# Kernel tuning notes

Measured on AMD Instinct MI355X. Metric: run time of the kernel, lower is better.

## Reference

```python
import jax, jax.numpy as jnp
import numpy as np

N_NODES = 100000
N_EDGES = 1600000
N_GRAPHS = 1024
HID = 128
NODE_DIM = 7
EDGE_DIM = 3
LAYERS = 4
LN_EPS = 1e-5


def setup_inputs() -> dict:
    key = jax.random.key(0)
    ks = jax.random.split(key, 24)
    s = lambda i, shape, scale=0.05: (jax.random.normal(ks[i], shape, dtype=jnp.float32) * scale)
    x = jax.random.normal(ks[0], (N_NODES, NODE_DIM), dtype=jnp.float32)
    edge_index = jax.random.randint(ks[1], (2, N_EDGES), 0, N_NODES, dtype=jnp.int32)
    edge_attr = jax.random.normal(ks[2], (N_EDGES, EDGE_DIM), dtype=jnp.float32)
    batch = jnp.sort(jax.random.randint(ks[3], (N_NODES,), 0, N_GRAPHS, dtype=jnp.int32))
    return {
        'x': x, 'edge_index': edge_index, 'edge_attr': edge_attr, 'batch': batch,
        'inW': s(4, (NODE_DIM, HID)), 'inb': s(5, (HID,)),
        'edgeW': s(6, (LAYERS, EDGE_DIM, HID)), 'edgeb': s(7, (LAYERS, HID)),
        'w1': s(8, (LAYERS, HID, HID)), 'b1': s(9, (LAYERS, HID)),
        'w2': s(10, (LAYERS, HID, HID)), 'b2': s(11, (LAYERS, HID)),
        'gamma': jnp.ones((LAYERS, HID), dtype=jnp.float32),
        'beta': jnp.zeros((LAYERS, HID), dtype=jnp.float32),
        'fcW1': s(12, (HID, HID)), 'fcb1': s(13, (HID,)),
        'fcW2': s(14, (HID, HID // 2)), 'fcb2': s(15, (HID // 2,)),
        'fcW3': s(16, (HID // 2, 1)), 'fcb3': s(17, (1,)),
    }


def _layernorm(x, gamma, beta):
    mu = jnp.mean(x, axis=-1, keepdims=True)
    var = jnp.mean(jnp.square(x - mu), axis=-1, keepdims=True)
    return (x - mu) * jax.lax.rsqrt(var + LN_EPS) * gamma + beta


def reference(x, edge_index, edge_attr, batch, inW, inb, edgeW, edgeb,
              w1, b1, w2, b2, gamma, beta, fcW1, fcb1, fcW2, fcb2, fcW3, fcb3):
    src, dst = edge_index[0], edge_index[1]
    h = x @ inW + inb  # [N, HID]
    for l in range(LAYERS):
        e = edge_attr @ edgeW[l] + edgeb[l]              # [E, HID]
        msg = jax.nn.relu(h[src] + e)                    # gather + relu
        agg = jax.ops.segment_sum(msg, dst, num_segments=N_NODES)  # scatter-add
        g = agg + h                                      # (1+eps)*x_r with eps=0
        g = jax.nn.relu(g @ w1[l] + b1[l]) @ w2[l] + b2[l]  # GINE MLP
        h = _layernorm(h + jax.nn.relu(g), gamma[l], beta[l])  # residual + LN
    # global mean pool over graphs
    sums = jax.ops.segment_sum(h, batch, num_segments=N_GRAPHS)
    cnt = jax.ops.segment_sum(jnp.ones((h.shape[0],), h.dtype), batch, num_segments=N_GRAPHS)
    pooled = sums / jnp.maximum(cnt, 1.0)[:, None]
    # head (dropout is identity in eval)
    o = jax.nn.relu(pooled @ fcW1 + fcb1)
    o = jax.nn.relu(o @ fcW2 + fcb2)
    return o @ fcW3 + fcb3  # [N_GRAPHS, 1]
```

## Files before the change

### kernel.cpp

```cpp
#include <hip/hip_runtime.h>

#define N_NODES 100000
#define N_EDGES 1600000
#define N_GRAPHS 1024
#define HID 128
#define LAYERS 4
#define LN_EPS 1e-5f
#define GTS 136
#define HLS 132
#define NB_PROJ 50000
#define NB_WCONV 512
#define NBUCK 1563
#define BCAP 2048
#define EPB 4096
#define NB_BS 391


typedef __attribute__((ext_vector_type(8))) short bf16x8;
typedef __attribute__((ext_vector_type(4))) float f32x4;
typedef __attribute__((ext_vector_type(2))) float f32x2;

__device__ __forceinline__ unsigned short f2bf(float x) {
    unsigned v = __float_as_uint(x);
    return (unsigned short)((v + 0x7fffu + ((v >> 16) & 1u)) >> 16);
}
__device__ __forceinline__ float bfval(unsigned short u) {
    return __uint_as_float((unsigned)u << 16);
}
__device__ __forceinline__ f32x2 pk_fma(f32x2 a, f32x2 b, f32x2 c) {
    f32x2 d;
    asm("v_pk_fma_f32 %0, %1, %2, %3" : "=v"(d) : "v"(a), "v"(b), "v"(c));
    return d;
}
__device__ __forceinline__ f32x2 pk_add(f32x2 a, f32x2 b) {
    f32x2 d;
    asm("v_pk_add_f32 %0, %1, %2" : "=v"(d) : "v"(a), "v"(b));
    return d;
}

__global__ __launch_bounds__(256) void k_prep(
    const float* __restrict__ x, const float* __restrict__ inW,
    const float* __restrict__ inb, float* __restrict__ h,
    unsigned short* __restrict__ hb,
    const float* __restrict__ w1, const float* __restrict__ w2,
    unsigned short* __restrict__ wf_hi, unsigned short* __restrict__ wf_lo,
    const int* __restrict__ ei, int* __restrict__ Xpb) {
    const int t = threadIdx.x;
    if (blockIdx.x < NB_BS) {
        __shared__ int hcnt[NBUCK];
        for (int i = t; i < NBUCK; i += 256) hcnt[i] = 0;
        __syncthreads();
        const int e0 = blockIdx.x * EPB;
        const int eend = (e0 + EPB < N_EDGES) ? e0 + EPB : N_EDGES;
#pragma unroll
        for (int k = 0; k < 16; ++k) {
            const int e = e0 + k * 256 + t;
            if (e < eend) atomicAdd(&hcnt[ei[N_EDGES + e] >> 6], 1);
        }
        __syncthreads();
        for (int i = t; i < NBUCK; i += 256)
            Xpb[blockIdx.x * NBUCK + i] = hcnt[i];
    } else if (blockIdx.x < NB_BS + NB_PROJ) {
        int idx = (blockIdx.x - NB_BS) * 256 + t;
        int n = idx >> 7, c = idx & 127;
        const float* xr = x + n * 7;
        float s = inb[c];
#pragma unroll
        for (int k = 0; k < 7; ++k) s += xr[k] * inW[k * HID + c];
        h[idx] = s;
        hb[idx] = f2bf(s);
    } else {
        int idx = (blockIdx.x - NB_BS - NB_PROJ) * 256 + t;
        int wid = idx >> 14;
        int layer = wid >> 1, which = wid & 1;
        int within = idx & 16383;
        int nt = within >> 11;
        int ks = (within >> 9) & 3;
        int ln = (within >> 3) & 63;
        int j = within & 7;
        const float* W = (which ? w2 : w1) + layer * HID * HID;
        int k = ks * 32 + (ln >> 4) * 8 + j;
        int n = nt * 16 + (ln & 15);
        float v = W[k * HID + n];
        unsigned short hi = f2bf(v);
        wf_hi[idx] = hi;
        wf_lo[idx] = f2bf(v - bfval(hi));
    }
}

__global__ __launch_bounds__(512) void k_bscan(
    const int* __restrict__ Xpb, int* __restrict__ lexcl,
    int* __restrict__ T) {
    __shared__ int tmp[512];
    const int b = blockIdx.x;
    const int t = threadIdx.x;
    int blk = -1;
    if (t < 343)        blk = (t % 49) * 8 + (t / 49);
    else if (t < NB_BS) blk = (t - 343) * 8 + 7;
    const int v = (blk >= 0) ? Xpb[blk * NBUCK + b] : 0;
    tmp[t] = v;
    __syncthreads();
    for (int off = 1; off < 512; off <<= 1) {
        const int u = (t >= off) ? tmp[t - off] : 0;
        __syncthreads();
        tmp[t] += u;
        __syncthreads();
    }
    if (blk >= 0) lexcl[b * NB_BS + blk] = tmp[t] - v;
    if (t == 511) T[b] = tmp[511];
}

__global__ __launch_bounds__(1024) void k_segscan(
    const int* __restrict__ T, int* __restrict__ bucket_base,
    int* __restrict__ row_ptr) {
    __shared__ int lsum[1024];
    const int t = threadIdx.x;
    const int b0 = 2 * t, b1 = 2 * t + 1;
    const int u0 = (b0 < NBUCK) ? T[b0] : 0;
    const int u1 = (b1 < NBUCK) ? T[b1] : 0;
    const int v = u0 + u1;
    lsum[t] = v;
    __syncthreads();
    for (int off = 1; off < 1024; off <<= 1) {
        const int u = (t >= off) ? lsum[t - off] : 0;
        __syncthreads();
        lsum[t] += u;
        __syncthreads();
    }
    const int excl = lsum[t] - v;
    if (b0 < NBUCK) bucket_base[b0] = excl;
    if (b1 < NBUCK) bucket_base[b1] = excl + u0;
    if (t == 0) {
        bucket_base[NBUCK] = N_EDGES;
        row_ptr[N_NODES] = N_EDGES;
    }
}

__global__ __launch_bounds__(256) void k_binscat(
    const int* __restrict__ ei, const float* __restrict__ ea,
    const int* __restrict__ bucket_base, const int* __restrict__ lexcl,
    int4* __restrict__ erec) {
    __shared__ int lcur[NBUCK];
    const int t = threadIdx.x;
    const int blk = blockIdx.x;
    for (int i = t; i < NBUCK; i += 256)
        lcur[i] = bucket_base[i] + lexcl[i * NB_BS + blk];
    __syncthreads();
    const int e0 = blk * EPB;
    const int eend = (e0 + EPB < N_EDGES) ? e0 + EPB : N_EDGES;
#pragma unroll
    for (int k = 0; k < 16; ++k) {
        const int e = e0 + k * 256 + t;
        if (e < eend) {
            const int src = ei[e];
            const int dst = ei[N_EDGES + e];
            const float a0 = ea[e * 3 + 0];
            const float a1 = ea[e * 3 + 1];
            const float a2 = ea[e * 3 + 2];
            const int pos = atomicAdd(&lcur[dst >> 6], 1);
            int4 r;
            r.x = src | ((dst & 63) << 20);
            r.y = __float_as_int(a0);
            r.z = __float_as_int(a1);
            r.w = __float_as_int(a2);
            erec[pos] = r;
        }
    }
}

__global__ __launch_bounds__(256) void k_bucketsort(
    const int4* __restrict__ erec, const int* __restrict__ bucket_base,
    int* __restrict__ row_ptr, int4* __restrict__ edata) {
    __shared__ int rhist[64];
    __shared__ int lcur[64];
    __shared__ int4 stage[BCAP];
    const int b = blockIdx.x;
    const int nb0 = b << 6;
    const int nrows = (nb0 + 64 <= N_NODES) ? 64 : (N_NODES - nb0);
    const int base = bucket_base[b];
    const int end = bucket_base[b + 1];
    const int cnt = end - base;
    const int t = threadIdx.x;
    if (t < 64) rhist[t] = 0;
    __syncthreads();
    for (int i = t; i < cnt; i += 256)
        atomicAdd(&rhist[(erec[base + i].x >> 20) & 63], 1);
    __syncthreads();
    if (t < 64) {
        const int v = rhist[t];
        int incl = v;
#pragma unroll
        for (int off = 1; off < 64; off <<= 1) {
            const int u = __shfl_up(incl, off);
            if (t >= off) incl += u;
        }
        const int excl = incl - v;
        lcur[t] = excl;
        if (t < nrows) row_ptr[nb0 + t] = base + excl;
    }
    __syncthreads();
    if (cnt <= BCAP) {
        for (int i = t; i < cnt; i += 256) {
            const int4 r = erec[base + i];
            stage[atomicAdd(&lcur[(r.x >> 20) & 63], 1)] = r;
        }
        __syncthreads();
        for (int i = t; i < cnt; i += 256) {
            int4 r = stage[i];
            r.x &= 0xFFFFF;
            edata[base + i] = r;
        }
    } else {
        for (int i = t; i < cnt; i += 256) {
            const int4 r = erec[base + i];
            const int pos = base + atomicAdd(&lcur[(r.x >> 20) & 63], 1);
            int4 o = r;
            o.x = r.x & 0xFFFFF;
            edata[pos] = o;
        }
    }
}

#define FLUSHSTEP {                                                            \
    if (rcur == 0)      { a0v = acc2; rnext = rp2; }                           \
    else if (rcur == 1) { a1v = acc2; rnext = rp3; }                           \
    else                { a2v = acc2; rnext = 0x7fffffff; }                    \
    acc2[0] = 0.f; acc2[1] = 0.f; ++rcur; }

#define EL(JJ)                                                                 \
    const int s##JJ = __builtin_amdgcn_readlane(cS, j + JJ);                   \
    const unsigned gq##JJ = *(const unsigned*)(hbin + (long)s##JJ * HID + c2);

#define EC(JJ) {                                                               \
    const int gi = t + j + (JJ);                                               \
    while (gi >= rnext) FLUSHSTEP                                              \
    const f32x4 qq = attAB[j + (JJ)];                                          \
    const f32x2 pC = attC[j + (JJ)];                                           \
    f32x2 pA; pA[0] = qq[0]; pA[1] = qq[1];                                    \
    f32x2 pB; pB[0] = qq[2]; pB[1] = qq[3];                                    \
    f32x2 g2; g2[0] = __uint_as_float(gq##JJ << 16);                           \
    g2[1] = __uint_as_float(gq##JJ & 0xffff0000u);                             \
    const f32x2 m2 = pk_fma(pC, ew2v, pk_fma(pB, ew1v, pk_fma(pA, ew0v,        \
                            pk_add(g2, ebv2))));                               \
    f32x2 r2; r2[0] = fmaxf(m2[0], 0.f); r2[1] = fmaxf(m2[1], 0.f);            \
    acc2 = pk_add(acc2, r2); }

#define ROW_OUT(R, AV) {                                                       \
    const float2 hv = *(const float2*)(h + (long)(nb + (R)) * HID + c2);       \
    *(float2*)&h_lds[(r0 + (R)) * HLS + c2] = hv;                              \
    const float gx = hv.x + (AV)[0], gy = hv.y + (AV)[1];                      \
    const unsigned short hx = f2bf(gx), hy = f2bf(gy);                         \
    const unsigned short lx = f2bf(gx - bfval(hx)), ly = f2bf(gy - bfval(hy)); \
    *(unsigned*)&gt_hi[(r0 + (R)) * GTS + c2] = (unsigned)hx | ((unsigned)hy << 16); \
    *(unsigned*)&gt_lo[(r0 + (R)) * GTS + c2] = (unsigned)lx | ((unsigned)ly << 16); }

#define T1_OUT(CC, NT) {                                                       \
    const float4 bv = *(const float4*)(b1 + (NT) * 16 + q4);                   \
    const float v0 = fmaxf(CC[0] + bv.x, 0.f);                                 \
    const float v1 = fmaxf(CC[1] + bv.y, 0.f);                                 \
    const float v2 = fmaxf(CC[2] + bv.z, 0.f);                                 \
    const float v3 = fmaxf(CC[3] + bv.w, 0.f);                                 \
    const unsigned short h0_ = f2bf(v0), h1_ = f2bf(v1), h2_ = f2bf(v2), h3_ = f2bf(v3); \
    const unsigned short l0_ = f2bf(v0 - bfval(h0_)), l1_ = f2bf(v1 - bfval(h1_)); \
    const unsigned short l2_ = f2bf(v2 - bfval(h2_)), l3_ = f2bf(v3 - bfval(h3_)); \
    *(uint2*)&t1_hi[ln15 * GTS + (NT) * 16 + q4] =                             \
        make_uint2((unsigned)h0_ | ((unsigned)h1_ << 16), (unsigned)h2_ | ((unsigned)h3_ << 16)); \
    *(uint2*)&t1_lo[ln15 * GTS + (NT) * 16 + q4] =                             \
        make_uint2((unsigned)l0_ | ((unsigned)l1_ << 16), (unsigned)l2_ | ((unsigned)l3_ << 16)); }

__global__ __launch_bounds__(256, 8) void k_node_update(
    const int4* __restrict__ edata, const int* __restrict__ row_ptr,
    const float* __restrict__ eW, const float* __restrict__ eb,
    float* __restrict__ h, const unsigned short* __restrict__ hbin,
    unsigned short* __restrict__ hbout,
    const unsigned short* __restrict__ w1f_hi, const unsigned short* __restrict__ w1f_lo,
    const unsigned short* __restrict__ w2f_hi, const unsigned short* __restrict__ w2f_lo,
    const float* __restrict__ b1, const float* __restrict__ b2,
    const float* __restrict__ gamma, const float* __restrict__ beta,
    const int write_hb) {
    __shared__ __align__(16) unsigned char smem[25856];
    float* stats = (float*)smem;
    unsigned short* gt_hi = (unsigned short*)(smem + 0);
    unsigned short* gt_lo = (unsigned short*)(smem + 4352);
    unsigned short* t1_hi = (unsigned short*)(smem + 8704);
    unsigned short* t1_lo = (unsigned short*)(smem + 13056);
    float* h_lds = (float*)(smem + 17408);

    const int wave = threadIdx.x >> 6;
    const int lane = threadIdx.x & 63;
    const int n0 = blockIdx.x * 16;
    const int r0 = wave * 4;
    const int c2 = lane * 2;

    {
        f32x4* attAB = (f32x4*)(smem + 8704 + wave * 1536);
        f32x2* attC  = (f32x2*)(smem + 8704 + wave * 1536 + 1024);
        const f32x2 ew0v = *(const f32x2*)(eW + 0 * HID + c2);
        const f32x2 ew1v = *(const f32x2*)(eW + 1 * HID + c2);
        const f32x2 ew2v = *(const f32x2*)(eW + 2 * HID + c2);
        const f32x2 ebv2 = *(const f32x2*)(eb + c2);
        const int nb = n0 + r0;
        const int rp0 = __builtin_amdgcn_readfirstlane(row_ptr[nb + 0]);
        const int rp1 = __builtin_amdgcn_readfirstlane(row_ptr[nb + 1]);
        const int rp2 = __builtin_amdgcn_readfirstlane(row_ptr[nb + 2]);
        const int rp3 = __builtin_amdgcn_readfirstlane(row_ptr[nb + 3]);
        const int rp4 = __builtin_amdgcn_readfirstlane(row_ptr[nb + 4]);

        f32x2 a0v = {0.f, 0.f}, a1v = {0.f, 0.f};
        f32x2 a2v = {0.f, 0.f}, a3v = {0.f, 0.f};
        f32x2 acc2 = {0.f, 0.f};
        int rcur = 0;
        int rnext = rp1;

        int4 cE = {0, 0, 0, 0}, nE = {0, 0, 0, 0};
        if (rp0 + lane < rp4) cE = edata[rp0 + lane];
        for (int t = rp0; t < rp4; t += 64) {
            const int cnt = (rp4 - t < 64) ? (rp4 - t) : 64;
            f32x4 dAB;
            dAB[0] = __int_as_float(cE.y); dAB[1] = dAB[0];
            dAB[2] = __int_as_float(cE.z); dAB[3] = dAB[2];
            f32x2 dC;
            dC[0] = __int_as_float(cE.w); dC[1] = dC[0];
            attAB[lane] = dAB;
            attC[lane] = dC;
            const int cS = cE.x;
            __builtin_amdgcn_wave_barrier();
            if (t + 64 + lane < rp4)
                nE = edata[t + 64 + lane];
            int j = 0;
            for (; j + 16 <= cnt; j += 16) {
                EL(0) EL(1) EL(2) EL(3) EL(4) EL(5) EL(6) EL(7)
                EL(8) EL(9) EL(10) EL(11) EL(12) EL(13) EL(14) EL(15)
                EC(0) EC(1) EC(2) EC(3) EC(4) EC(5) EC(6) EC(7)
                EC(8) EC(9) EC(10) EC(11) EC(12) EC(13) EC(14) EC(15)
            }
            for (; j + 4 <= cnt; j += 4) {
                EL(0) EL(1) EL(2) EL(3)
                EC(0) EC(1) EC(2) EC(3)
            }
            for (; j < cnt; ++j) {
                EL(0)
                EC(0)
            }
            __builtin_amdgcn_wave_barrier();
            cE = nE;
        }
        if (rcur == 0)      a0v = acc2;
        else if (rcur == 1) a1v = acc2;
        else if (rcur == 2) a2v = acc2;
        else                a3v = acc2;
        ROW_OUT(0, a0v)
        ROW_OUT(1, a1v)
        ROW_OUT(2, a2v)
        ROW_OUT(3, a3v)
    }
    __syncthreads();

    const int ln15 = lane & 15;
    const int q8 = (lane >> 4) * 8;
    const int q4 = (lane >> 4) * 4;
    const int nt0 = wave * 2, nt1 = nt0 + 1;

    {
        f32x4 c0 = {0.f, 0.f, 0.f, 0.f};
        f32x4 c1 = {0.f, 0.f, 0.f, 0.f};
#pragma unroll
        for (int ks = 0; ks < 4; ++ks) {
            const bf16x8 bh = *(const bf16x8*)&gt_hi[ln15 * GTS + ks * 32 + q8];
            const bf16x8 bl = *(const bf16x8*)&gt_lo[ln15 * GTS + ks * 32 + q8];
            const bf16x8 a0h = *(const bf16x8*)(w1f_hi + (((nt0 * 4 + ks) * 64 + lane) << 3));
            const bf16x8 a0l = *(const bf16x8*)(w1f_lo + (((nt0 * 4 + ks) * 64 + lane) << 3));
            const bf16x8 a1h = *(const bf16x8*)(w1f_hi + (((nt1 * 4 + ks) * 64 + lane) << 3));
            const bf16x8 a1l = *(const bf16x8*)(w1f_lo + (((nt1 * 4 + ks) * 64 + lane) << 3));
            c0 = __builtin_amdgcn_mfma_f32_16x16x32_bf16(a0h, bh, c0, 0, 0, 0);
            c0 = __builtin_amdgcn_mfma_f32_16x16x32_bf16(a0h, bl, c0, 0, 0, 0);
            c0 = __builtin_amdgcn_mfma_f32_16x16x32_bf16(a0l, bh, c0, 0, 0, 0);
            c1 = __builtin_amdgcn_mfma_f32_16x16x32_bf16(a1h, bh, c1, 0, 0, 0);
            c1 = __builtin_amdgcn_mfma_f32_16x16x32_bf16(a1h, bl, c1, 0, 0, 0);
            c1 = __builtin_amdgcn_mfma_f32_16x16x32_bf16(a1l, bh, c1, 0, 0, 0);
        }
        T1_OUT(c0, nt0)
        T1_OUT(c1, nt1)
    }
    __syncthreads();

    {
        f32x4 c0 = {0.f, 0.f, 0.f, 0.f};
        f32x4 c1 = {0.f, 0.f, 0.f, 0.f};
#pragma unroll
        for (int ks = 0; ks < 4; ++ks) {
            const bf16x8 bh = *(const bf16x8*)&t1_hi[ln15 * GTS + ks * 32 + q8];
            const bf16x8 bl = *(const bf16x8*)&t1_lo[ln15 * GTS + ks * 32 + q8];
            const bf16x8 a0h = *(const bf16x8*)(w2f_hi + (((nt0 * 4 + ks) * 64 + lane) << 3));
            const bf16x8 a0l = *(const bf16x8*)(w2f_lo + (((nt0 * 4 + ks) * 64 + lane) << 3));
            const bf16x8 a1h = *(const bf16x8*)(w2f_hi + (((nt1 * 4 + ks) * 64 + lane) << 3));
            const bf16x8 a1l = *(const bf16x8*)(w2f_lo + (((nt1 * 4 + ks) * 64 + lane) << 3));
            c0 = __builtin_amdgcn_mfma_f32_16x16x32_bf16(a0h, bh, c0, 0, 0, 0);
            c0 = __builtin_amdgcn_mfma_f32_16x16x32_bf16(a0h, bl, c0, 0, 0, 0);
            c0 = __builtin_amdgcn_mfma_f32_16x16x32_bf16(a0l, bh, c0, 0, 0, 0);
            c1 = __builtin_amdgcn_mfma_f32_16x16x32_bf16(a1h, bh, c1, 0, 0, 0);
            c1 = __builtin_amdgcn_mfma_f32_16x16x32_bf16(a1h, bl, c1, 0, 0, 0);
            c1 = __builtin_amdgcn_mfma_f32_16x16x32_bf16(a1l, bh, c1, 0, 0, 0);
        }
        const int row = n0 + ln15;
        const float4 b20 = *(const float4*)(b2 + nt0 * 16 + q4);
        const float4 b21 = *(const float4*)(b2 + nt1 * 16 + q4);
        const float4 hv0 = *(const float4*)&h_lds[ln15 * HLS + nt0 * 16 + q4];
        const float4 hv1 = *(const float4*)&h_lds[ln15 * HLS + nt1 * 16 + q4];
        float4 u0, u1;
        u0.x = hv0.x + fmaxf(c0[0] + b20.x, 0.f);
        u0.y = hv0.y + fmaxf(c0[1] + b20.y, 0.f);
        u0.z = hv0.z + fmaxf(c0[2] + b20.z, 0.f);
        u0.w = hv0.w + fmaxf(c0[3] + b20.w, 0.f);
        u1.x = hv1.x + fmaxf(c1[0] + b21.x, 0.f);
        u1.y = hv1.y + fmaxf(c1[1] + b21.y, 0.f);
        u1.z = hv1.z + fmaxf(c1[2] + b21.z, 0.f);
        u1.w = hv1.w + fmaxf(c1[3] + b21.w, 0.f);
        float s = u0.x + u0.y + u0.z + u0.w + u1.x + u1.y + u1.z + u1.w;
        float s2 = u0.x * u0.x + u0.y * u0.y + u0.z * u0.z + u0.w * u0.w +
                   u1.x * u1.x + u1.y * u1.y + u1.z * u1.z + u1.w * u1.w;
        s += __shfl_xor(s, 16); s2 += __shfl_xor(s2, 16);
        s += __shfl_xor(s, 32); s2 += __shfl_xor(s2, 32);
        if (lane < 16) {
            stats[wave * 32 + lane * 2 + 0] = s;
            stats[wave * 32 + lane * 2 + 1] = s2;
        }
        __syncthreads();
        const float S  = stats[0 * 32 + ln15 * 2] + stats[1 * 32 + ln15 * 2] +
                         stats[2 * 32 + ln15 * 2] + stats[3 * 32 + ln15 * 2];
        const float S2 = stats[0 * 32 + ln15 * 2 + 1] + stats[1 * 32 + ln15 * 2 + 1] +
                         stats[2 * 32 + ln15 * 2 + 1] + stats[3 * 32 + ln15 * 2 + 1];
        const float mu = S * (1.f / HID);
        const float var = S2 * (1.f / HID) - mu * mu;
        const float inv = rsqrtf(var + LN_EPS);
        const float4 gm0 = *(const float4*)(gamma + nt0 * 16 + q4);
        const float4 gm1 = *(const float4*)(gamma + nt1 * 16 + q4);
        const float4 bt0 = *(const float4*)(beta + nt0 * 16 + q4);
        const float4 bt1 = *(const float4*)(beta + nt1 * 16 + q4);
        float4 o0, o1;
        o0.x = (u0.x - mu) * inv * gm0.x + bt0.x;
        o0.y = (u0.y - mu) * inv * gm0.y + bt0.y;
        o0.z = (u0.z - mu) * inv * gm0.z + bt0.z;
        o0.w = (u0.w - mu) * inv * gm0.w + bt0.w;
        o1.x = (u1.x - mu) * inv * gm1.x + bt1.x;
        o1.y = (u1.y - mu) * inv * gm1.y + bt1.y;
        o1.z = (u1.z - mu) * inv * gm1.z + bt1.z;
        o1.w = (u1.w - mu) * inv * gm1.w + bt1.w;
        *(float4*)(h + (long)row * HID + nt0 * 16 + q4) = o0;
        *(float4*)(h + (long)row * HID + nt1 * 16 + q4) = o1;
        if (write_hb) {
            *(uint2*)(hbout + (long)row * HID + nt0 * 16 + q4) =
                make_uint2((unsigned)f2bf(o0.x) | ((unsigned)f2bf(o0.y) << 16),
                           (unsigned)f2bf(o0.z) | ((unsigned)f2bf(o0.w) << 16));
            *(uint2*)(hbout + (long)row * HID + nt1 * 16 + q4) =
                make_uint2((unsigned)f2bf(o1.x) | ((unsigned)f2bf(o1.y) << 16),
                           (unsigned)f2bf(o1.z) | ((unsigned)f2bf(o1.w) << 16));
        }
    }
}

__global__ __launch_bounds__(128) void k_head(
    const float* __restrict__ h, const int* __restrict__ batch,
    const float* __restrict__ fcW1, const float* __restrict__ fcb1,
    const float* __restrict__ fcW2, const float* __restrict__ fcb2,
    const float* __restrict__ fcW3, const float* __restrict__ fcb3,
    float* __restrict__ out) {
    __shared__ float p[HID];
    __shared__ float o1[HID];
    __shared__ float o2[64];
    const int g = blockIdx.x, t = threadIdx.x;
    int lo = 0, hi = N_NODES;
    while (lo < hi) {
        const int m = (lo + hi) >> 1;
        if (batch[m] < g) lo = m + 1; else hi = m;
    }
    const int start = lo;
    hi = N_NODES;
    while (lo < hi) {
        const int m = (lo + hi) >> 1;
        if (batch[m] < g + 1) lo = m + 1; else hi = m;
    }
    const int end = lo;
    float acc = 0.f;
    for (int n = start; n < end; ++n) acc += h[(long)n * HID + t];
    const float c = fmaxf((float)(end - start), 1.0f);
    p[t] = acc / c;
    __syncthreads();
    float s = fcb1[t];
    for (int k = 0; k < HID; ++k) s += p[k] * fcW1[k * HID + t];
    o1[t] = fmaxf(s, 0.f);
    __syncthreads();
    if (t < 64) {
        float s2 = fcb2[t];
        for (int k = 0; k < HID; ++k) s2 += o1[k] * fcW2[k * 64 + t];
        o2[t] = fmaxf(s2, 0.f);
    }
    __syncthreads();
    if (t < 64) {
        float v = o2[t] * fcW3[t];
#pragma unroll
        for (int off = 32; off > 0; off >>= 1) v += __shfl_down(v, off);
        if (t == 0) out[g] = v + fcb3[0];
    }
}

extern "C" void kernel_launch(void* const* d_in, const int* in_sizes, int n_in,
                              void* d_out, int out_size, void* d_ws, size_t ws_size,
                              hipStream_t stream) {
    const float* x    = (const float*)d_in[0];
    const int*   ei   = (const int*)d_in[1];
    const float* ea   = (const float*)d_in[2];
    const int*   batch= (const int*)d_in[3];
    const float* inW  = (const float*)d_in[4];
    const float* inb  = (const float*)d_in[5];
    const float* edgeW= (const float*)d_in[6];
    const float* edgeb= (const float*)d_in[7];
    const float* w1   = (const float*)d_in[8];
    const float* b1   = (const float*)d_in[9];
    const float* w2   = (const float*)d_in[10];
    const float* b2   = (const float*)d_in[11];
    const float* gamma= (const float*)d_in[12];
    const float* beta = (const float*)d_in[13];
    const float* fcW1 = (const float*)d_in[14];
    const float* fcb1 = (const float*)d_in[15];
    const float* fcW2 = (const float*)d_in[16];
    const float* fcb2 = (const float*)d_in[17];
    const float* fcW3 = (const float*)d_in[18];
    const float* fcb3 = (const float*)d_in[19];
    float* out = (float*)d_out;

    int4*  edata = (int4*)d_ws;
    float* h     = (float*)(edata + (size_t)N_EDGES);
    unsigned short* hb0 = (unsigned short*)(h + (size_t)N_NODES * HID);
    unsigned short* hb1 = hb0 + (size_t)N_NODES * HID;
    unsigned short* wf_hi = hb1 + (size_t)N_NODES * HID;
    unsigned short* wf_lo = wf_hi + LAYERS * 2 * 16384;
    int*    row_ptr = (int*)(wf_lo + LAYERS * 2 * 16384);
    int*    bucket_base = row_ptr + (N_NODES + 1);
    int*    T       = bucket_base + (NBUCK + 1);
    int*    Xpb     = (int*)edata;
    int*    lexcl   = Xpb + (size_t)NB_BS * NBUCK;
    int4*   erec    = (int4*)hb1;

    k_prep<<<NB_BS + NB_PROJ + NB_WCONV, 256, 0, stream>>>(
        x, inW, inb, h, hb0, w1, w2, wf_hi, wf_lo, ei, Xpb);

    k_bscan<<<NBUCK, 512, 0, stream>>>(Xpb, lexcl, T);
    k_segscan<<<1, 1024, 0, stream>>>(T, bucket_base, row_ptr);
    k_binscat<<<NB_BS, 256, 0, stream>>>(ei, ea, bucket_base, lexcl, erec);
    k_bucketsort<<<NBUCK, 256, 0, stream>>>(erec, bucket_base, row_ptr, edata);

    unsigned short* hbin = hb0;
    unsigned short* hbout = hb1;
    for (int l = 0; l < LAYERS; ++l) {
        k_node_update<<<N_NODES / 16, 256, 0, stream>>>(
            edata, row_ptr, edgeW + l * 3 * HID, edgeb + l * HID,
            h, hbin, hbout,
            wf_hi + (l * 2 + 0) * 16384, wf_lo + (l * 2 + 0) * 16384,
            wf_hi + (l * 2 + 1) * 16384, wf_lo + (l * 2 + 1) * 16384,
            b1 + l * HID, b2 + l * HID, gamma + l * HID, beta + l * HID,
            (l < LAYERS - 1) ? 1 : 0);
        unsigned short* tmp = hbin; hbin = hbout; hbout = tmp;
    }

    k_head<<<N_GRAPHS, 128, 0, stream>>>(h, batch, fcW1, fcb1, fcW2, fcb2,
                                         fcW3, fcb3, out);
}
```

Measured before the change: 636.7 us.

## Batch bucket scan with wave shuffles and drop h staging in node-update LDS

Rewrites k_bscan so each 256-thread block scans 16 buckets at once. It loads the per-block counts coalesced into padded LDS and scans them with 64-lane shuffle prefix sums instead of a 512-thread barrier-heavy Hillis-Steele scan. The lexcl layout becomes block-major, so k_binscat reads its row contiguously. In k_node_update the h row is no longer staged in LDS, cutting shared memory from about 25.8 KB to 17 KB for higher occupancy, at the cost of re-reading h from global (likely cached) in the epilogue.

```diff
diff --git a/kernel.cpp b/kernel.cpp
--- a/kernel.cpp
+++ b/kernel.cpp
@@ -7,13 +7,14 @@
 #define LAYERS 4
 #define LN_EPS 1e-5f
 #define GTS 136
-#define HLS 132
 #define NB_PROJ 50000
 #define NB_WCONV 512
 #define NBUCK 1563
 #define BCAP 2048
 #define EPB 4096
 #define NB_BS 391
+#define BSB 16
+#define BSP 17
 
 
 typedef __attribute__((ext_vector_type(8))) short bf16x8;
@@ -88,26 +89,45 @@
     }
 }
 
-__global__ __launch_bounds__(512) void k_bscan(
+__global__ __launch_bounds__(256) void k_bscan(
     const int* __restrict__ Xpb, int* __restrict__ lexcl,
     int* __restrict__ T) {
-    __shared__ int tmp[512];
-    const int b = blockIdx.x;
+    __shared__ int xs[NB_BS * BSP];
+    const int b0 = blockIdx.x * BSB;
     const int t = threadIdx.x;
-    int blk = -1;
-    if (t < 343)        blk = (t % 49) * 8 + (t / 49);
-    else if (t < NB_BS) blk = (t - 343) * 8 + 7;
-    const int v = (blk >= 0) ? Xpb[blk * NBUCK + b] : 0;
-    tmp[t] = v;
-    __syncthreads();
-    for (int off = 1; off < 512; off <<= 1) {
-        const int u = (t >= off) ? tmp[t - off] : 0;
-        __syncthreads();
-        tmp[t] += u;
-        __syncthreads();
-    }
-    if (blk >= 0) lexcl[b * NB_BS + blk] = tmp[t] - v;
-    if (t == 511) T[b] = tmp[511];
+    for (int idx = t; idx < NB_BS * BSB; idx += 256) {
+        const int p = idx >> 4, c = idx & 15;
+        const int blk = (p < 343) ? (p % 49) * 8 + p / 49 : (p - 343) * 8 + 7;
+        const int b = b0 + c;
+        xs[p * BSP + c] = (b < NBUCK) ? Xpb[blk * NBUCK + b] : 0;
+    }
+    __syncthreads();
+    const int wave = t >> 6, lane = t & 63;
+#pragma unroll
+    for (int cc = 0; cc < 4; ++cc) {
+        const int c = wave * 4 + cc;
+        int run = 0;
+        for (int tile = 0; tile < 7; ++tile) {
+            const int p = tile * 64 + lane;
+            const int v = (p < NB_BS) ? xs[p * BSP + c] : 0;
+            int incl = v;
+#pragma unroll
+            for (int off = 1; off < 64; off <<= 1) {
+                const int u = __shfl_up(incl, off);
+                if (lane >= off) incl += u;
+            }
+            if (p < NB_BS) xs[p * BSP + c] = run + incl - v;
+            run += __shfl(incl, 63);
+        }
+        if (lane == 0 && b0 + c < NBUCK) T[b0 + c] = run;
+    }
+    __syncthreads();
+    for (int idx = t; idx < NB_BS * BSB; idx += 256) {
+        const int p = idx >> 4, c = idx & 15;
+        const int blk = (p < 343) ? (p % 49) * 8 + p / 49 : (p - 343) * 8 + 7;
+        const int b = b0 + c;
+        if (b < NBUCK) lexcl[blk * NBUCK + b] = xs[p * BSP + c];
+    }
 }
 
 __global__ __launch_bounds__(1024) void k_segscan(
@@ -143,8 +163,9 @@
     __shared__ int lcur[NBUCK];
     const int t = threadIdx.x;
     const int blk = blockIdx.x;
+    const int* lrow = lexcl + (size_t)blk * NBUCK;
     for (int i = t; i < NBUCK; i += 256)
-        lcur[i] = bucket_base[i] + lexcl[i * NB_BS + blk];
+        lcur[i] = bucket_base[i] + lrow[i];
     __syncthreads();
     const int e0 = blk * EPB;
     const int eend = (e0 + EPB < N_EDGES) ? e0 + EPB : N_EDGES;
@@ -247,7 +268,6 @@
 
 #define ROW_OUT(R, AV) {                                                       \
     const float2 hv = *(const float2*)(h + (long)(nb + (R)) * HID + c2);       \
-    *(float2*)&h_lds[(r0 + (R)) * HLS + c2] = hv;                              \
     const float gx = hv.x + (AV)[0], gy = hv.y + (AV)[1];                      \
     const unsigned short hx = f2bf(gx), hy = f2bf(gy);                         \
     const unsigned short lx = f2bf(gx - bfval(hx)), ly = f2bf(gy - bfval(hy)); \
@@ -278,13 +298,12 @@
     const float* __restrict__ b1, const float* __restrict__ b2,
     const float* __restrict__ gamma, const float* __restrict__ beta,
     const int write_hb) {
-    __shared__ __align__(16) unsigned char smem[25856];
+    __shared__ __align__(16) unsigned char smem[17408];
     float* stats = (float*)smem;
     unsigned short* gt_hi = (unsigned short*)(smem + 0);
     unsigned short* gt_lo = (unsigned short*)(smem + 4352);
     unsigned short* t1_hi = (unsigned short*)(smem + 8704);
     unsigned short* t1_lo = (unsigned short*)(smem + 13056);
-    float* h_lds = (float*)(smem + 17408);
 
     const int wave = threadIdx.x >> 6;
     const int lane = threadIdx.x & 63;
@@ -405,8 +424,8 @@
         const int row = n0 + ln15;
         const float4 b20 = *(const float4*)(b2 + nt0 * 16 + q4);
         const float4 b21 = *(const float4*)(b2 + nt1 * 16 + q4);
-        const float4 hv0 = *(const float4*)&h_lds[ln15 * HLS + nt0 * 16 + q4];
-        const float4 hv1 = *(const float4*)&h_lds[ln15 * HLS + nt1 * 16 + q4];
+        const float4 hv0 = *(const float4*)(h + (long)row * HID + nt0 * 16 + q4);
+        const float4 hv1 = *(const float4*)(h + (long)row * HID + nt1 * 16 + q4);
         float4 u0, u1;
         u0.x = hv0.x + fmaxf(c0[0] + b20.x, 0.f);
         u0.y = hv0.y + fmaxf(c0[1] + b20.y, 0.f);
@@ -545,7 +564,7 @@
     k_prep<<<NB_BS + NB_PROJ + NB_WCONV, 256, 0, stream>>>(
         x, inW, inb, h, hb0, w1, w2, wf_hi, wf_lo, ei, Xpb);
 
-    k_bscan<<<NBUCK, 512, 0, stream>>>(Xpb, lexcl, T);
+    k_bscan<<<(NBUCK + BSB - 1) / BSB, 256, 0, stream>>>(Xpb, lexcl, T);
     k_segscan<<<1, 1024, 0, stream>>>(T, bucket_base, row_ptr);
     k_binscat<<<NB_BS, 256, 0, stream>>>(ei, ea, bucket_base, lexcl, erec);
     k_bucketsort<<<NBUCK, 256, 0, stream>>>(erec, bucket_base, row_ptr, edata);
```

Result: slower. 656.2 us, median of 2 (+3.1%).
